# Performance work log

Measured on AMD Instinct MI355X. Metric: run time of the kernel, lower is better.

Reference implementation:

```python
import jax, jax.numpy as jnp
import numpy as np
from jax import lax

N, T, D_IN = 8192, 64, 64
R = 256            # reservoir_dim
K = 3              # diffusion hops
D_OUT = 64
E = 131072
LEAK = 0.3
SPECTRAL_RADIUS = 0.9
SPARSITY = 0.9


def setup_inputs() -> dict:
    key = jax.random.key(0)
    kx, ke = jax.random.split(key)
    rng = np.random.default_rng(0)

    # ESN fixed buffers (match torch init: randn*0.1; sparse randn scaled to rho)
    W_in = (rng.standard_normal((R, D_IN)) * 0.1).astype(np.float32)
    W_res = rng.standard_normal((R, R)).astype(np.float32)
    mask = rng.random((R, R)) < SPARSITY
    W_res[mask] = 0.0
    rho = float(np.abs(np.linalg.eigvals(W_res)).max())
    if rho > 1e-8:
        W_res = W_res * (SPECTRAL_RADIUS / rho)

    # readout: Linear((K+1)*R -> 2*D_OUT), GELU, Linear(2*D_OUT -> D_OUT), LayerNorm
    fan1 = (K + 1) * R
    W1 = (rng.standard_normal((2 * D_OUT, fan1)) / np.sqrt(fan1)).astype(np.float32)
    b1 = np.zeros((2 * D_OUT,), np.float32)
    W2 = (rng.standard_normal((D_OUT, 2 * D_OUT)) / np.sqrt(2 * D_OUT)).astype(np.float32)
    b2 = np.zeros((D_OUT,), np.float32)
    gamma = np.ones((D_OUT,), np.float32)
    beta = np.zeros((D_OUT,), np.float32)

    x = jax.random.normal(kx, (N, T, D_IN), dtype=jnp.float32)
    edge_index = jax.random.randint(ke, (2, E), 0, N, dtype=jnp.int64)

    return {
        "x": x,
        "edge_index": edge_index,
        "W_in": jnp.asarray(W_in),
        "W_res": jnp.asarray(W_res),
        "W1": jnp.asarray(W1), "b1": jnp.asarray(b1),
        "W2": jnp.asarray(W2), "b2": jnp.asarray(b2),
        "gamma": jnp.asarray(gamma), "beta": jnp.asarray(beta),
    }


def _esn(x, W_in, W_res):
    # x: [N, T, D_IN] -> final reservoir state [N, R]
    x_proj = jnp.einsum("ntd,rd->tnr", x, W_in)  # [T, N, R]

    def step(h, xp_t):
        h_new = jnp.tanh(xp_t + h @ W_res.T)
        return (1.0 - LEAK) * h + LEAK * h_new, None

    h0 = jnp.zeros((x.shape[0], W_res.shape[0]), dtype=x.dtype)
    h, _ = lax.scan(step, h0, x_proj)
    return h


def _norm_adj(edge_index, n_nodes):
    # symmetric D^{-1/2} A D^{-1/2}; dedup handled by idempotent .set
    row = jnp.concatenate([edge_index[0], edge_index[1]])
    col = jnp.concatenate([edge_index[1], edge_index[0]])
    A_bin = jnp.zeros((n_nodes, n_nodes), jnp.float32).at[row, col].set(1.0)
    deg = A_bin.sum(axis=1)
    dinv = jnp.where(deg > 0, 1.0 / jnp.sqrt(jnp.maximum(deg, 1e-12)), 0.0)
    dinv = jnp.minimum(dinv, 1e6)
    return dinv[:, None] * A_bin * dinv[None, :]


def reference(x, edge_index, W_in, W_res, W1, b1, W2, b2, gamma, beta):
    h = _esn(x, W_in, W_res)                    # [N, R]
    A = _norm_adj(edge_index, x.shape[0])       # [N, N]

    diffused = [h]
    h_k = h
    for _ in range(K):
        h_k = A @ h_k
        diffused.append(h_k)
    cat = jnp.concatenate(diffused, axis=-1)    # [N, (K+1)*R]

    z = jax.nn.gelu(cat @ W1.T + b1, approximate=False)
    z = z @ W2.T + b2                           # [N, D_OUT]
    mu = z.mean(axis=-1, keepdims=True)
    var = z.var(axis=-1, keepdims=True)
    z = (z - mu) / jnp.sqrt(var + 1e-5)
    return z * gamma + beta
```

## Files before the change

kernel.cpp:

```cpp
#include <hip/hip_runtime.h>
#include <hip/hip_bf16.h>
#include <hip/hip_fp16.h>
#include <math.h>

#define NN    8192
#define TT    64
#define DIN   64
#define RR    256
#define DOUT  64
#define HID   128
#define CATD  1024
#define NE    131072
#define MASKW 256
#define MAXD  256
#define HROW  328

typedef __attribute__((ext_vector_type(8))) short    s16x8;
typedef __attribute__((ext_vector_type(8))) _Float16 f16x8;
typedef __attribute__((ext_vector_type(4))) float    f32x4;

static __device__ __forceinline__ unsigned short f2bs(float f) {
  union { __hip_bfloat16 b; unsigned short u; } cv;
  cv.b = __float2bfloat16(f);
  return cv.u;
}
static __device__ __forceinline__ unsigned int pack2bf(float a, float b) {
  return (unsigned int)f2bs(a) | ((unsigned int)f2bs(b) << 16);
}
static __device__ __forceinline__ unsigned int pack2h(float a, float b) {
  return (unsigned int)__half_as_ushort(__float2half(a))
       | ((unsigned int)__half_as_ushort(__float2half(b)) << 16);
}
static __device__ __forceinline__ float fast_tanh(float v) {
  float e = __builtin_amdgcn_exp2f(v * 2.8853900817779268f);
  return 1.0f - 2.0f * __builtin_amdgcn_rcpf(e + 1.0f);
}


__global__ __launch_bounds__(256) void zero_mask_kernel(uint4* mask4, int n4) {
  int i = blockIdx.x * 256 + threadIdx.x;
  if (i < n4) mask4[i] = make_uint4(0u, 0u, 0u, 0u);
}

__global__ __launch_bounds__(256) void edge_kernel(const int* __restrict__ eidx,
                                                   unsigned int* __restrict__ mask) {
  int e = blockIdx.x * 256 + threadIdx.x;
  if (e < NE) {
    int u = eidx[e];
    int v = eidx[NE + e];
    atomicOr(&mask[(size_t)u * MASKW + (v >> 5)], 1u << (v & 31));
    atomicOr(&mask[(size_t)v * MASKW + (u >> 5)], 1u << (u & 31));
  }
}

__global__ __launch_bounds__(256) void nbrlist_kernel(const unsigned int* __restrict__ mask,
                                                      unsigned short* __restrict__ nbrlist,
                                                      int* __restrict__ nbrcnt,
                                                      float* __restrict__ dinv) {
  __shared__ int wsum[4];
  const int n = blockIdx.x;
  const int tid = threadIdx.x;
  const int lane = tid & 63;
  const int w = tid >> 6;
  unsigned int m = mask[(size_t)n * MASKW + tid];
  const int c = __popc(m);
  int inc = c;
#pragma unroll
  for (int d = 1; d < 64; d <<= 1) {
    int v = __shfl_up(inc, d, 64);
    if (lane >= d) inc += v;
  }
  if (lane == 63) wsum[w] = inc;
  __syncthreads();
  int base = 0;
  for (int i = 0; i < w; ++i) base += wsum[i];
  int off = base + inc - c;
  while (m) {
    int b = __ffs(m) - 1;
    m &= m - 1;
    if (off < MAXD) nbrlist[(size_t)n * MAXD + off] = (unsigned short)(tid * 32 + b);
    ++off;
  }
  if (tid == 255) {
    int tot = base + inc;
    nbrcnt[n] = tot < MAXD ? tot : MAXD;
    dinv[n] = (tot > 0) ? fminf(rsqrtf((float)tot), 1e6f) : 0.0f;
  }
}

__global__ __launch_bounds__(256) void cvt_weights_kernel(
    const float* __restrict__ Wres, const float* __restrict__ Win,
    const float* __restrict__ W1, const float* __restrict__ W2,
    unsigned short* __restrict__ wresh, unsigned short* __restrict__ winh,
    unsigned short* __restrict__ W1h, unsigned short* __restrict__ W2h) {
  int i = blockIdx.x * 256 + threadIdx.x;
  if (i < 65536) wresh[i] = f2bs(Wres[i]);
  else if (i < 81920) winh[i - 65536] = f2bs(Win[i - 65536]);
  else if (i < 212992) W1h[i - 81920] = __half_as_ushort(__float2half(W1[i - 81920]));
  else if (i < 221184) W2h[i - 212992] = __half_as_ushort(__float2half(W2[i - 212992]));
}

__global__ __launch_bounds__(512, 4) void esn_mfma_kernel(
    const float* __restrict__ x,
    const unsigned short* __restrict__ winh,
    const unsigned short* __restrict__ wresh,
    unsigned short* __restrict__ cat)
{
  __shared__ unsigned short hs[2][16][HROW];
  const int tid  = threadIdx.x;
  const int lane = tid & 63;
  const int w    = tid >> 6;
  const int lr   = lane & 15;
  const int lg   = lane >> 4;
  const int sn   = tid >> 5;
  const int sq   = tid & 31;
  const long gn0 = (long)blockIdx.x * 16;
  const int bx   = (lr >> 3) & 1;
  const int lgx  = lg ^ bx;
  const int lgw  = (lg >> 1) ^ bx;
  const int bs   = (sn >> 3) & 1;

  s16x8 waug[2][10];
#pragma unroll
  for (int rt = 0; rt < 2; ++rt) {
    const int r = w * 32 + rt * 16 + lr;
#pragma unroll
    for (int kt = 0; kt < 8; ++kt)
      waug[rt][kt] = *(const s16x8*)(wresh + r * RR + kt * 32 + lg * 8);
#pragma unroll
    for (int kt = 8; kt < 10; ++kt)
      waug[rt][kt] = *(const s16x8*)(winh + r * DIN + (kt - 8) * 32 + lg * 8);
  }

  unsigned short* const rd0 = &hs[0][0][0] + lr * HROW + lgx * 8;
  unsigned short* const rd1 = &hs[1][0][0] + lr * HROW + lgx * 8;
  unsigned short* const wh0 = &hs[0][0][0] + lr * HROW + (w * 4 + lgw) * 8 + (lg & 1) * 4;
  unsigned short* const wh1 = &hs[1][0][0] + lr * HROW + (w * 4 + lgw) * 8 + (lg & 1) * 4;
  unsigned short* const xs0 = &hs[0][0][0] + sn * HROW + (32 + ((sq >> 2) ^ bs)) * 8 + (sq & 3) * 2;
  unsigned short* const xs1 = &hs[1][0][0] + sn * HROW + (32 + ((sq >> 2) ^ bs)) * 8 + (sq & 3) * 2;

  for (int i = tid; i < 16 * HROW / 2; i += 512) ((unsigned int*)hs[0])[i] = 0u;

  const float* xrow = x + (gn0 + sn) * (long)(TT * DIN) + sq * 2;
  float2 xr0 = *(const float2*)(xrow);
  float2 xr1 = *(const float2*)(xrow + DIN);
  __syncthreads();
  *(unsigned int*)xs0 = pack2bf(xr0.x, xr0.y);
  xr0 = *(const float2*)(xrow + 2 * DIN);

  f32x4 hreg[2];
  hreg[0] = (f32x4){0.f, 0.f, 0.f, 0.f};
  hreg[1] = (f32x4){0.f, 0.f, 0.f, 0.f};
  __syncthreads();

#define ESN_STEP(RD, WH, XS, XRS, XRL, TNEXT)                                        \
  {                                                                                  \
    f32x4 a0e = (f32x4){0.f,0.f,0.f,0.f}, a0o = a0e, a1e = a0e, a1o = a0e;           \
    _Pragma("unroll")                                                                \
    for (int kt = 0; kt < 10; kt += 2) {                                             \
      const s16x8 hbe = *(const s16x8*)(RD + kt * 32);                               \
      const s16x8 hbo = *(const s16x8*)(RD + (kt + 1) * 32);                         \
      a0e = __builtin_amdgcn_mfma_f32_16x16x32_bf16(waug[0][kt], hbe, a0e, 0, 0, 0); \
      a1e = __builtin_amdgcn_mfma_f32_16x16x32_bf16(waug[1][kt], hbe, a1e, 0, 0, 0); \
      a0o = __builtin_amdgcn_mfma_f32_16x16x32_bf16(waug[0][kt+1], hbo, a0o, 0, 0, 0);\
      a1o = __builtin_amdgcn_mfma_f32_16x16x32_bf16(waug[1][kt+1], hbo, a1o, 0, 0, 0);\
    }                                                                                \
    *(unsigned int*)(XS) = pack2bf(XRS.x, XRS.y);                 \
    XRL = *(const float2*)(xrow + (TNEXT) * DIN);                      \
    _Pragma("unroll")                                                                \
    for (int rt = 0; rt < 2; ++rt) {                                                 \
      const f32x4 ae = rt ? a1e : a0e;                                               \
      const f32x4 ao = rt ? a1o : a0o;                                               \
      f32x4 hn;                                                                      \
      _Pragma("unroll")                                                              \
      for (int i = 0; i < 4; ++i)                                                    \
        hn[i] = 0.7f * hreg[rt][i] + 0.3f * fast_tanh(ae[i] + ao[i]);                \
      hreg[rt] = hn;                                                                 \
      *(uint2*)(WH + rt * 16) =                                                      \
          make_uint2(pack2bf(hn[0], hn[1]), pack2bf(hn[2], hn[3]));                  \
    }                                                                                \
  }

  for (int tc = 0; tc < TT / 2; ++tc) {
    const int t = tc * 2;
    const int tla = (t + 3 < TT) ? t + 3 : TT - 1;
    ESN_STEP(rd0, wh1, xs1, xr1, xr1, tla);
    __syncthreads();
    const int tlb = (t + 4 < TT) ? t + 4 : TT - 1;
    ESN_STEP(rd1, wh0, xs0, xr0, xr0, tlb);
    __syncthreads();
  }
#undef ESN_STEP

#pragma unroll
  for (int rt = 0; rt < 2; ++rt) {
    *(uint2*)(cat + (gn0 + lr) * CATD + w * 32 + rt * 16 + lg * 4) =
        make_uint2(pack2h(hreg[rt][0], hreg[rt][1]), pack2h(hreg[rt][2], hreg[rt][3]));
  }
}

__global__ __launch_bounds__(256) void spmv_kernel(
    const unsigned short* __restrict__ nbrlist, const int* __restrict__ nbrcnt,
    const float* __restrict__ dinv, unsigned short* __restrict__ cat, int hop)
{
  const int wv   = threadIdx.x >> 6;
  const int lane = threadIdx.x & 63;
  const int n    = blockIdx.x * 4 + wv;
  const int cnt  = nbrcnt[n];
  const __half* in = (const __half*)cat + (size_t)(hop - 1) * RR;
  float4 acc = make_float4(0.f, 0.f, 0.f, 0.f);
  for (int c0 = 0; c0 < cnt; c0 += 64) {
    const int m = (cnt - c0 < 64) ? cnt - c0 : 64;
    int idx = 0; float dv = 0.f;
    if (lane < m) {
      idx = (int)nbrlist[(size_t)n * MAXD + c0 + lane];
      dv  = dinv[idx];
    }
#pragma unroll 4
    for (int i = 0; i < m; ++i) {
      const int   j  = __builtin_amdgcn_readfirstlane(__shfl(idx, i, 64));
      const float wj = __shfl(dv, i, 64);
      const uint2 u  = *(const uint2*)(in + (size_t)j * CATD + lane * 4);
      const __half2 h01 = *(const __half2*)&u.x;
      const __half2 h23 = *(const __half2*)&u.y;
      const float2 f01 = __half22float2(h01);
      const float2 f23 = __half22float2(h23);
      acc.x += wj * f01.x; acc.y += wj * f01.y;
      acc.z += wj * f23.x; acc.w += wj * f23.y;
    }
  }
  const float dn = dinv[n];
  *(uint2*)(cat + (size_t)n * CATD + (size_t)hop * RR + lane * 4) =
      make_uint2(pack2h(acc.x * dn, acc.y * dn), pack2h(acc.z * dn, acc.w * dn));
}

__global__ __launch_bounds__(256) void readout_kernel(
    const unsigned short* __restrict__ cat,
    const unsigned short* __restrict__ W1h,
    const float* __restrict__ b1,
    const unsigned short* __restrict__ W2h,
    const float* __restrict__ b2, const float* __restrict__ gamma,
    const float* __restrict__ beta, float* __restrict__ out)
{
  __shared__ unsigned short z1[16][136];
  __shared__ float z2[16][68];
  const int tid  = threadIdx.x;
  const int lane = tid & 63;
  const int w    = tid >> 6;
  const int lr   = lane & 15;
  const int lg   = lane >> 4;
  const long gn0 = (long)blockIdx.x * 16;

  f32x4 a0 = (f32x4){0.f, 0.f, 0.f, 0.f};
  f32x4 a1 = (f32x4){0.f, 0.f, 0.f, 0.f};
  const unsigned short* arow  = cat + (gn0 + lr) * CATD;
  const unsigned short* b0row = W1h + (w * 32 + lr) * CATD;
  const unsigned short* b1row = W1h + (w * 32 + 16 + lr) * CATD;
#pragma unroll 8
  for (int kt = 0; kt < 32; ++kt) {
    const f16x8 af  = *(const f16x8*)(arow  + kt * 32 + lg * 8);
    const f16x8 bf0 = *(const f16x8*)(b0row + kt * 32 + lg * 8);
    const f16x8 bf1 = *(const f16x8*)(b1row + kt * 32 + lg * 8);
    a0 = __builtin_amdgcn_mfma_f32_16x16x32_f16(af, bf0, a0, 0, 0, 0);
    a1 = __builtin_amdgcn_mfma_f32_16x16x32_f16(af, bf1, a1, 0, 0, 0);
  }
  const float is2 = 0.70710678118654752f;
#pragma unroll
  for (int nt = 0; nt < 2; ++nt) {
    const int hid = w * 32 + nt * 16 + lr;
    const float bb = b1[hid];
    const f32x4 a = nt ? a1 : a0;
#pragma unroll
    for (int i = 0; i < 4; ++i) {
      const float v = a[i] + bb;
      const float g = 0.5f * v * (1.0f + erff(v * is2));
      z1[lg * 4 + i][hid] = __half_as_ushort(__float2half(g));
    }
  }
  __syncthreads();

  f32x4 c2 = (f32x4){0.f, 0.f, 0.f, 0.f};
  const unsigned short* w2row = W2h + (w * 16 + lr) * HID;
#pragma unroll
  for (int kt = 0; kt < 4; ++kt) {
    const f16x8 af = *(const f16x8*)(&z1[lr][kt * 32 + lg * 8]);
    const f16x8 bf = *(const f16x8*)(w2row + kt * 32 + lg * 8);
    c2 = __builtin_amdgcn_mfma_f32_16x16x32_f16(af, bf, c2, 0, 0, 0);
  }
  {
    const float bb = b2[w * 16 + lr];
#pragma unroll
    for (int i = 0; i < 4; ++i) z2[lg * 4 + i][w * 16 + lr] = c2[i] + bb;
  }
  __syncthreads();

  {
    const int n = tid >> 4;
    const int c = tid & 15;
    const float v0 = z2[n][c], v1 = z2[n][c + 16], v2 = z2[n][c + 32], v3 = z2[n][c + 48];
    float s  = v0 + v1 + v2 + v3;
    float s2 = v0 * v0 + v1 * v1 + v2 * v2 + v3 * v3;
#pragma unroll
    for (int m = 1; m < 16; m <<= 1) {
      s  += __shfl_xor(s,  m, 64);
      s2 += __shfl_xor(s2, m, 64);
    }
    const float mu  = s * (1.0f / 64.0f);
    const float var = s2 * (1.0f / 64.0f) - mu * mu;
    const float inv = rsqrtf(var + 1e-5f);
    float* orow = out + (gn0 + n) * DOUT;
    orow[c]      = (v0 - mu) * inv * gamma[c]      + beta[c];
    orow[c + 16] = (v1 - mu) * inv * gamma[c + 16] + beta[c + 16];
    orow[c + 32] = (v2 - mu) * inv * gamma[c + 32] + beta[c + 32];
    orow[c + 48] = (v3 - mu) * inv * gamma[c + 48] + beta[c + 48];
  }
}


extern "C" void kernel_launch(void* const* d_in, const int* in_sizes, int n_in,
                              void* d_out, int out_size, void* d_ws, size_t ws_size,
                              hipStream_t stream) {
  const float* x     = (const float*)d_in[0];
  const int*   eidx  = (const int*)d_in[1];
  const float* W_in  = (const float*)d_in[2];
  const float* W_res = (const float*)d_in[3];
  const float* W1    = (const float*)d_in[4];
  const float* b1    = (const float*)d_in[5];
  const float* W2    = (const float*)d_in[6];
  const float* b2    = (const float*)d_in[7];
  const float* gamma = (const float*)d_in[8];
  const float* beta  = (const float*)d_in[9];
  float* out = (float*)d_out;

  char* ws = (char*)d_ws;
  size_t off = 0;
  auto alloc = [&](size_t bytes) {
    void* p = ws + off;
    off += (bytes + 255) & ~(size_t)255;
    return p;
  };
  unsigned int*   mask    = (unsigned int*)  alloc((size_t)NN * MASKW * 4);
  unsigned short* cat     = (unsigned short*)alloc((size_t)NN * CATD * 2);
  unsigned short* nbrlist = (unsigned short*)alloc((size_t)NN * MAXD * 2);
  int*            nbrcnt  = (int*)           alloc((size_t)NN * 4);
  float*          dinv    = (float*)         alloc((size_t)NN * 4);
  unsigned short* wresh   = (unsigned short*)alloc((size_t)RR * RR * 2);
  unsigned short* winh    = (unsigned short*)alloc((size_t)RR * DIN * 2);
  unsigned short* W1h     = (unsigned short*)alloc((size_t)HID * CATD * 2);
  unsigned short* W2h     = (unsigned short*)alloc((size_t)DOUT * HID * 2);

  zero_mask_kernel<<<2048, 256, 0, stream>>>((uint4*)mask, NN * MASKW / 4);
  edge_kernel<<<NE / 256, 256, 0, stream>>>(eidx, mask);
  nbrlist_kernel<<<NN, 256, 0, stream>>>(mask, nbrlist, nbrcnt, dinv);
  cvt_weights_kernel<<<864, 256, 0, stream>>>(W_res, W_in, W1, W2, wresh, winh, W1h, W2h);

  esn_mfma_kernel<<<NN / 16, 512, 0, stream>>>(x, winh, wresh, cat);

  for (int k = 1; k <= 3; ++k)
    spmv_kernel<<<NN / 4, 256, 0, stream>>>(nbrlist, nbrcnt, dinv, cat, k);

  readout_kernel<<<NN / 16, 256, 0, stream>>>(cat, W1h, b1, W2h, b2, gamma, beta, out);
}
```

Baseline: 197.3 us.

## Retile spmv to half-wave per node, double readout rows per block, tweak ESN step

```diff
diff --git a/kernel.cpp b/kernel.cpp
--- a/kernel.cpp
+++ b/kernel.cpp
@@ -30,10 +30,6 @@
 static __device__ __forceinline__ unsigned int pack2h(float a, float b) {
   return (unsigned int)__half_as_ushort(__float2half(a))
        | ((unsigned int)__half_as_ushort(__float2half(b)) << 16);
-}
-static __device__ __forceinline__ float fast_tanh(float v) {
-  float e = __builtin_amdgcn_exp2f(v * 2.8853900817779268f);
-  return 1.0f - 2.0f * __builtin_amdgcn_rcpf(e + 1.0f);
 }
 
 
@@ -156,6 +152,7 @@
 #define ESN_STEP(RD, WH, XS, XRS, XRL, TNEXT)                                        \
   {                                                                                  \
     f32x4 a0e = (f32x4){0.f,0.f,0.f,0.f}, a0o = a0e, a1e = a0e, a1o = a0e;           \
+    __builtin_amdgcn_s_setprio(1);                                                   \
     _Pragma("unroll")                                                                \
     for (int kt = 0; kt < 10; kt += 2) {                                             \
       const s16x8 hbe = *(const s16x8*)(RD + kt * 32);                               \
@@ -165,6 +162,7 @@
       a0o = __builtin_amdgcn_mfma_f32_16x16x32_bf16(waug[0][kt+1], hbo, a0o, 0, 0, 0);\
       a1o = __builtin_amdgcn_mfma_f32_16x16x32_bf16(waug[1][kt+1], hbo, a1o, 0, 0, 0);\
     }                                                                                \
+    __builtin_amdgcn_s_setprio(0);                                                   \
     *(unsigned int*)(XS) = pack2bf(XRS.x, XRS.y);                 \
     XRL = *(const float2*)(xrow + (TNEXT) * DIN);                      \
     _Pragma("unroll")                                                                \
@@ -173,8 +171,12 @@
       const f32x4 ao = rt ? a1o : a0o;                                               \
       f32x4 hn;                                                                      \
       _Pragma("unroll")                                                              \
-      for (int i = 0; i < 4; ++i)                                                    \
-        hn[i] = 0.7f * hreg[rt][i] + 0.3f * fast_tanh(ae[i] + ao[i]);                \
+      for (int i = 0; i < 4; ++i) {                                                  \
+        const float sacc = ae[i] + ao[i];                                            \
+        const float e = __builtin_amdgcn_exp2f(sacc * 2.8853900817779268f);          \
+        const float rc = __builtin_amdgcn_rcpf(e + 1.0f);                            \
+        hn[i] = fmaf(-0.6f, rc, fmaf(0.7f, hreg[rt][i], 0.3f));                      \
+      }                                                                              \
       hreg[rt] = hn;                                                                 \
       *(uint2*)(WH + rt * 16) =                                                      \
           make_uint2(pack2bf(hn[0], hn[1]), pack2bf(hn[2], hn[3]));                  \
@@ -205,33 +207,44 @@
 {
   const int wv   = threadIdx.x >> 6;
   const int lane = threadIdx.x & 63;
-  const int n    = blockIdx.x * 4 + wv;
+  const int half = lane >> 5;
+  const int li   = lane & 31;
+  const int n    = blockIdx.x * 8 + wv * 2 + half;
   const int cnt  = nbrcnt[n];
   const __half* in = (const __half*)cat + (size_t)(hop - 1) * RR;
-  float4 acc = make_float4(0.f, 0.f, 0.f, 0.f);
-  for (int c0 = 0; c0 < cnt; c0 += 64) {
-    const int m = (cnt - c0 < 64) ? cnt - c0 : 64;
+  float acc[8];
+#pragma unroll
+  for (int k = 0; k < 8; ++k) acc[k] = 0.0f;
+
+  for (int c0 = 0; c0 < cnt; c0 += 32) {
+    const int m = (cnt - c0 < 32) ? cnt - c0 : 32;
     int idx = 0; float dv = 0.f;
-    if (lane < m) {
-      idx = (int)nbrlist[(size_t)n * MAXD + c0 + lane];
+    if (li < m) {
+      idx = (int)nbrlist[(size_t)n * MAXD + c0 + li];
       dv  = dinv[idx];
     }
-#pragma unroll 4
+#pragma unroll 8
     for (int i = 0; i < m; ++i) {
-      const int   j  = __builtin_amdgcn_readfirstlane(__shfl(idx, i, 64));
-      const float wj = __shfl(dv, i, 64);
-      const uint2 u  = *(const uint2*)(in + (size_t)j * CATD + lane * 4);
-      const __half2 h01 = *(const __half2*)&u.x;
-      const __half2 h23 = *(const __half2*)&u.y;
-      const float2 f01 = __half22float2(h01);
-      const float2 f23 = __half22float2(h23);
-      acc.x += wj * f01.x; acc.y += wj * f01.y;
-      acc.z += wj * f23.x; acc.w += wj * f23.y;
+      const int   j  = __shfl(idx, half * 32 + i, 64);
+      const float wj = __shfl(dv,  half * 32 + i, 64);
+      const uint4 u  = *(const uint4*)(in + (size_t)j * CATD + li * 8);
+      const float2 f0 = __half22float2(*(const __half2*)&u.x);
+      const float2 f1 = __half22float2(*(const __half2*)&u.y);
+      const float2 f2 = __half22float2(*(const __half2*)&u.z);
+      const float2 f3 = __half22float2(*(const __half2*)&u.w);
+      acc[0] += wj * f0.x; acc[1] += wj * f0.y;
+      acc[2] += wj * f1.x; acc[3] += wj * f1.y;
+      acc[4] += wj * f2.x; acc[5] += wj * f2.y;
+      acc[6] += wj * f3.x; acc[7] += wj * f3.y;
     }
   }
   const float dn = dinv[n];
-  *(uint2*)(cat + (size_t)n * CATD + (size_t)hop * RR + lane * 4) =
-      make_uint2(pack2h(acc.x * dn, acc.y * dn), pack2h(acc.z * dn, acc.w * dn));
+  uint4 o;
+  o.x = pack2h(acc[0] * dn, acc[1] * dn);
+  o.y = pack2h(acc[2] * dn, acc[3] * dn);
+  o.z = pack2h(acc[4] * dn, acc[5] * dn);
+  o.w = pack2h(acc[6] * dn, acc[7] * dn);
+  *(uint4*)(cat + (size_t)n * CATD + (size_t)hop * RR + li * 8) = o;
 }
 
 __global__ __launch_bounds__(256) void readout_kernel(
@@ -242,66 +255,80 @@
     const float* __restrict__ b2, const float* __restrict__ gamma,
     const float* __restrict__ beta, float* __restrict__ out)
 {
-  __shared__ unsigned short z1[16][136];
-  __shared__ float z2[16][68];
+  __shared__ unsigned short z1[32][136];
+  __shared__ float z2[32][68];
   const int tid  = threadIdx.x;
   const int lane = tid & 63;
   const int w    = tid >> 6;
   const int lr   = lane & 15;
   const int lg   = lane >> 4;
-  const long gn0 = (long)blockIdx.x * 16;
-
-  f32x4 a0 = (f32x4){0.f, 0.f, 0.f, 0.f};
-  f32x4 a1 = (f32x4){0.f, 0.f, 0.f, 0.f};
-  const unsigned short* arow  = cat + (gn0 + lr) * CATD;
-  const unsigned short* b0row = W1h + (w * 32 + lr) * CATD;
-  const unsigned short* b1row = W1h + (w * 32 + 16 + lr) * CATD;
+  const long gn0 = (long)blockIdx.x * 32;
+
+  f32x4 a00 = (f32x4){0.f,0.f,0.f,0.f}, a01 = a00, a10 = a00, a11 = a00;
+  const unsigned short* arow0 = cat + (gn0 + lr) * CATD;
+  const unsigned short* arow1 = cat + (gn0 + 16 + lr) * CATD;
+  const unsigned short* brow0 = W1h + (w * 32 + lr) * CATD;
+  const unsigned short* brow1 = W1h + (w * 32 + 16 + lr) * CATD;
 #pragma unroll 8
   for (int kt = 0; kt < 32; ++kt) {
-    const f16x8 af  = *(const f16x8*)(arow  + kt * 32 + lg * 8);
-    const f16x8 bf0 = *(const f16x8*)(b0row + kt * 32 + lg * 8);
-    const f16x8 bf1 = *(const f16x8*)(b1row + kt * 32 + lg * 8);
-    a0 = __builtin_amdgcn_mfma_f32_16x16x32_f16(af, bf0, a0, 0, 0, 0);
-    a1 = __builtin_amdgcn_mfma_f32_16x16x32_f16(af, bf1, a1, 0, 0, 0);
+    const f16x8 af0 = *(const f16x8*)(arow0 + kt * 32 + lg * 8);
+    const f16x8 af1 = *(const f16x8*)(arow1 + kt * 32 + lg * 8);
+    const f16x8 bf0 = *(const f16x8*)(brow0 + kt * 32 + lg * 8);
+    const f16x8 bf1 = *(const f16x8*)(brow1 + kt * 32 + lg * 8);
+    a00 = __builtin_amdgcn_mfma_f32_16x16x32_f16(af0, bf0, a00, 0, 0, 0);
+    a01 = __builtin_amdgcn_mfma_f32_16x16x32_f16(af0, bf1, a01, 0, 0, 0);
+    a10 = __builtin_amdgcn_mfma_f32_16x16x32_f16(af1, bf0, a10, 0, 0, 0);
+    a11 = __builtin_amdgcn_mfma_f32_16x16x32_f16(af1, bf1, a11, 0, 0, 0);
   }
   const float is2 = 0.70710678118654752f;
 #pragma unroll
   for (int nt = 0; nt < 2; ++nt) {
-    const int hid = w * 32 + nt * 16 + lr;
-    const float bb = b1[hid];
-    const f32x4 a = nt ? a1 : a0;
-#pragma unroll
-    for (int i = 0; i < 4; ++i) {
-      const float v = a[i] + bb;
-      const float g = 0.5f * v * (1.0f + erff(v * is2));
-      z1[lg * 4 + i][hid] = __half_as_ushort(__float2half(g));
-    }
-  }
-  __syncthreads();
-
-  f32x4 c2 = (f32x4){0.f, 0.f, 0.f, 0.f};
+#pragma unroll
+    for (int ht = 0; ht < 2; ++ht) {
+      const int hid = w * 32 + ht * 16 + lr;
+      const float bb = b1[hid];
+      const f32x4 a = nt ? (ht ? a11 : a10) : (ht ? a01 : a00);
+#pragma unroll
+      for (int i = 0; i < 4; ++i) {
+        const float v = a[i] + bb;
+        const float g = 0.5f * v * (1.0f + erff(v * is2));
+        z1[nt * 16 + lg * 4 + i][hid] = __half_as_ushort(__float2half(g));
+      }
+    }
+  }
+  __syncthreads();
+
+  f32x4 c20 = (f32x4){0.f,0.f,0.f,0.f}, c21 = c20;
   const unsigned short* w2row = W2h + (w * 16 + lr) * HID;
 #pragma unroll
   for (int kt = 0; kt < 4; ++kt) {
-    const f16x8 af = *(const f16x8*)(&z1[lr][kt * 32 + lg * 8]);
-    const f16x8 bf = *(const f16x8*)(w2row + kt * 32 + lg * 8);
-    c2 = __builtin_amdgcn_mfma_f32_16x16x32_f16(af, bf, c2, 0, 0, 0);
+    const f16x8 bf  = *(const f16x8*)(w2row + kt * 32 + lg * 8);
+    const f16x8 af0 = *(const f16x8*)(&z1[lr][kt * 32 + lg * 8]);
+    const f16x8 af1 = *(const f16x8*)(&z1[16 + lr][kt * 32 + lg * 8]);
+    c20 = __builtin_amdgcn_mfma_f32_16x16x32_f16(af0, bf, c20, 0, 0, 0);
+    c21 = __builtin_amdgcn_mfma_f32_16x16x32_f16(af1, bf, c21, 0, 0, 0);
   }
   {
     const float bb = b2[w * 16 + lr];
 #pragma unroll
-    for (int i = 0; i < 4; ++i) z2[lg * 4 + i][w * 16 + lr] = c2[i] + bb;
+    for (int i = 0; i < 4; ++i) {
+      z2[lg * 4 + i][w * 16 + lr]      = c20[i] + bb;
+      z2[16 + lg * 4 + i][w * 16 + lr] = c21[i] + bb;
+    }
   }
   __syncthreads();
 
   {
-    const int n = tid >> 4;
-    const int c = tid & 15;
-    const float v0 = z2[n][c], v1 = z2[n][c + 16], v2 = z2[n][c + 32], v3 = z2[n][c + 48];
-    float s  = v0 + v1 + v2 + v3;
-    float s2 = v0 * v0 + v1 * v1 + v2 * v2 + v3 * v3;
-#pragma unroll
-    for (int m = 1; m < 16; m <<= 1) {
+    const int n = tid >> 3;
+    const int c = tid & 7;
+    float v[8], s = 0.0f, s2 = 0.0f;
+#pragma unroll
+    for (int k2 = 0; k2 < 8; ++k2) {
+      v[k2] = z2[n][c + 8 * k2];
+      s += v[k2]; s2 += v[k2] * v[k2];
+    }
+#pragma unroll
+    for (int m = 1; m < 8; m <<= 1) {
       s  += __shfl_xor(s,  m, 64);
       s2 += __shfl_xor(s2, m, 64);
     }
@@ -309,10 +336,9 @@
     const float var = s2 * (1.0f / 64.0f) - mu * mu;
     const float inv = rsqrtf(var + 1e-5f);
     float* orow = out + (gn0 + n) * DOUT;
-    orow[c]      = (v0 - mu) * inv * gamma[c]      + beta[c];
-    orow[c + 16] = (v1 - mu) * inv * gamma[c + 16] + beta[c + 16];
-    orow[c + 32] = (v2 - mu) * inv * gamma[c + 32] + beta[c + 32];
-    orow[c + 48] = (v3 - mu) * inv * gamma[c + 48] + beta[c + 48];
+#pragma unroll
+    for (int k2 = 0; k2 < 8; ++k2)
+      orow[c + 8 * k2] = (v[k2] - mu) * inv * gamma[c + 8 * k2] + beta[c + 8 * k2];
   }
 }
 
@@ -357,7 +383,7 @@
   esn_mfma_kernel<<<NN / 16, 512, 0, stream>>>(x, winh, wresh, cat);
 
   for (int k = 1; k <= 3; ++k)
-    spmv_kernel<<<NN / 4, 256, 0, stream>>>(nbrlist, nbrcnt, dinv, cat, k);
-
-  readout_kernel<<<NN / 16, 256, 0, stream>>>(cat, W1h, b1, W2h, b2, gamma, beta, out);
-}
+    spmv_kernel<<<NN / 8, 256, 0, stream>>>(nbrlist, nbrcnt, dinv, cat, k);
+
+  readout_kernel<<<NN / 32, 256, 0, stream>>>(cat, W1h, b1, W2h, b2, gamma, beta, out);
+}
```

Result: faster. 193.0 us (-2.2%).
